# Optimization experiments

Hardware: AMD Instinct MI355X
Metric: run time of the kernel (lower is better)

Reference implementation:

```python
import jax, jax.numpy as jnp
import numpy as np

# Config: 4 sparse batch items, each with 2048 active voxels (uniform-length case
# of sparse full self-attention). channels=1024, heads=16, head_dim=64.
B_SEQ, L, H, D = 4, 2048, 16, 64
C = H * D  # 1024
N = B_SEQ * L  # 8192
EPS = 1e-12  # F.normalize eps


def setup_inputs() -> dict:
    key = jax.random.key(0)
    ks = jax.random.split(key, 6)
    s = 1.0 / np.sqrt(C)
    return {
        "x": jax.random.normal(ks[0], (N, C), dtype=jnp.float32),
        "W_qkv": jax.random.normal(ks[1], (C, 3 * C), dtype=jnp.float32) * s,
        "b_qkv": jnp.zeros((3 * C,), dtype=jnp.float32),
        "gamma_q": jnp.ones((H, D), dtype=jnp.float32),
        "gamma_k": jnp.ones((H, D), dtype=jnp.float32),
        "W_out": jax.random.normal(ks[2], (C, C), dtype=jnp.float32) * s,
        "b_out": jnp.zeros((C,), dtype=jnp.float32),
    }


def _qk_rms_norm(t, gamma):
    # SparseMultiHeadRMSNorm: L2-normalize last dim, scale by gamma[h,d] * sqrt(D)
    norm = jnp.maximum(jnp.linalg.norm(t, axis=-1, keepdims=True), EPS)
    return (t / norm) * gamma * (D ** 0.5)


def reference(x, W_qkv, b_qkv, gamma_q, gamma_k, W_out, b_out):
    qkv = x @ W_qkv + b_qkv                       # [N, 3C]
    qkv = qkv.reshape(B_SEQ, L, 3, H, D)          # fused pre-reshape
    q, k, v = qkv[:, :, 0], qkv[:, :, 1], qkv[:, :, 2]  # [B,L,H,D]
    q = _qk_rms_norm(q, gamma_q)
    k = _qk_rms_norm(k, gamma_k)
    # full scaled dot-product attention within each sparse batch item
    scores = jnp.einsum('blhd,bmhd->bhlm', q, k) / (D ** 0.5)
    attn = jax.nn.softmax(scores, axis=-1)
    h = jnp.einsum('bhlm,bmhd->blhd', attn, v)    # [B,L,H,D]
    h = h.reshape(N, C)
    return h @ W_out + b_out
```

## Files before the change

### kernel.cpp

```cpp
#include <hip/hip_runtime.h>

using u16 = unsigned short;

typedef float  f32x4  __attribute__((ext_vector_type(4)));
typedef float  f32x16 __attribute__((ext_vector_type(16)));
typedef __bf16 bf16x8 __attribute__((ext_vector_type(8)));
typedef short  s16x8  __attribute__((ext_vector_type(8)));

#define DEVI __device__ __forceinline__

constexpr int TOK = 8192;
constexpr int CIN = 1024;
constexpr int C3  = 3072;
constexpr int NH  = 16;
constexpr int HD  = 64;
constexpr int SL  = 2048;
constexpr int BH  = 64;

constexpr float LOG2E = 1.4426950408889634f;

DEVI u16 f2bf(float x) {
  unsigned u = __builtin_bit_cast(unsigned, x);
  u += 0x7FFFu + ((u >> 16) & 1u);
  return (u16)(u >> 16);
}

DEVI f32x4 mfma16(s16x8 a, s16x8 b, f32x4 c) {
  return __builtin_amdgcn_mfma_f32_16x16x32_bf16(
      __builtin_bit_cast(bf16x8, a), __builtin_bit_cast(bf16x8, b), c, 0, 0, 0);
}

DEVI f32x16 mfma32(s16x8 a, s16x8 b, f32x16 c) {
  return __builtin_amdgcn_mfma_f32_32x32x16_bf16(
      __builtin_bit_cast(bf16x8, a), __builtin_bit_cast(bf16x8, b), c, 0, 0, 0);
}

DEVI void gload_lds16(const void* g, void* l) {
  __builtin_amdgcn_global_load_lds(
      (const __attribute__((address_space(1))) unsigned int*)g,
      (__attribute__((address_space(3))) unsigned int*)l, 16, 0, 0);
}

DEVI unsigned cvtpk(float lo, float hi) {
  unsigned r;
  asm("v_cvt_pk_bf16_f32 %0, %1, %2" : "=v"(r) : "v"(lo), "v"(hi));
  return r;
}

DEVI void plswap(unsigned& a, unsigned& b) {
  asm("v_permlane32_swap_b32 %0, %1" : "+v"(a), "+v"(b));
}

DEVI void do_transpose(const float* __restrict__ in, u16* __restrict__ out,
                       int R, int C, int blk, int tid, u16 (*t)[72]) {
  int rt = R >> 6;
  int tr = (blk % rt) << 6;
  int tc = (blk / rt) << 6;
#pragma unroll
  for (int k2 = 0; k2 < 16; k2++) {
    int idx = k2 * 256 + tid;
    int r = idx >> 6, c = idx & 63;
    t[r][c] = f2bf(in[(size_t)(tr + r) * C + tc + c]);
  }
  __syncthreads();
#pragma unroll
  for (int k2 = 0; k2 < 16; k2++) {
    int idx = k2 * 256 + tid;
    int r = idx >> 6, c = idx & 63;
    out[(size_t)(tc + r) * R + tr + c] = t[c][r];
  }
}

__global__ __launch_bounds__(256) void k_prep(
    const float* __restrict__ x, u16* __restrict__ xb,
    const float* __restrict__ Wqkv, u16* __restrict__ wqT,
    const float* __restrict__ Wout, u16* __restrict__ woT,
    const float* __restrict__ gq, const float* __restrict__ gk,
    float* __restrict__ bnd) {
  __shared__ u16 t[64][72];
  const int bid = blockIdx.x, tid = threadIdx.x;
  if (bid < 1024) {
    const int total = TOK * CIN / 4;
    for (int i = bid * 256 + tid; i < total; i += 1024 * 256) {
      float4 v = ((const float4*)x)[i];
      ushort4 o;
      o.x = f2bf(v.x); o.y = f2bf(v.y); o.z = f2bf(v.z); o.w = f2bf(v.w);
      ((ushort4*)xb)[i] = o;
    }
  } else if (bid < 1024 + 768) {
    do_transpose(Wqkv, wqT, 1024, 3072, bid - 1024, tid, t);
  } else if (bid < 1024 + 768 + 256) {
    do_transpose(Wout, woT, 1024, 1024, bid - 1792, tid, t);
  } else {
    const int h = tid >> 4, s = tid & 15;
    float mv = 0.f;
#pragma unroll
    for (int j = 0; j < 4; j++) {
      int d = s * 4 + j;
      mv = fmaxf(mv, fabsf(gq[h * 64 + d] * gk[h * 64 + d]));
    }
    mv = fmaxf(mv, __shfl_xor(mv, 1));
    mv = fmaxf(mv, __shfl_xor(mv, 2));
    mv = fmaxf(mv, __shfl_xor(mv, 4));
    mv = fmaxf(mv, __shfl_xor(mv, 8));
    if (s == 0) bnd[h] = 8.0f * LOG2E * mv;
  }
}

#define STAGE6(BUF, KT)                                                  \
  { char* Ld = L + (BUF) * 49152;                                        \
    const size_t ko = (size_t)(KT) * 128;                                \
    gload_lds16(Ab + ko,          Ld + wb);                              \
    gload_lds16(Ab + ko + 131072, Ld + 8192 + wb);                       \
    gload_lds16(Ab + ko + 262144, Ld + 16384 + wb);                      \
    gload_lds16(Ab + ko + 393216, Ld + 24576 + wb);                      \
    gload_lds16(Bb + ko,          Ld + 32768 + wb);                      \
    gload_lds16(Bb + ko + 131072, Ld + 40960 + wb); }

#define KBODY(KT, DOSTAGE, VMSTR)                                        \
  {                                                                      \
    if (DOSTAGE) STAGE6(((KT) + 2) % 3, (KT) + 2)                        \
    asm volatile("s_waitcnt " VMSTR ::: "memory");                       \
    __builtin_amdgcn_s_barrier();                                        \
    const char* Lb = L + ((KT) % 3) * 49152;                             \
    s16x8 af[4][2], bfr[4][2];                                           \
    _Pragma("unroll")                                                    \
    for (int mf = 0; mf < 4; mf++) {                                     \
      af[mf][0] = *(const s16x8*)(Lb + aoff + mf * 2048 + cx0);          \
      af[mf][1] = *(const s16x8*)(Lb + aoff + mf * 2048 + (cx0 ^ 64));   \
    }                                                                    \
    _Pragma("unroll")                                                    \
    for (int nf = 0; nf < 4; nf++) {                                     \
      bfr[nf][0] = *(const s16x8*)(Lb + boff + nf * 2048 + cx0);         \
      bfr[nf][1] = *(const s16x8*)(Lb + boff + nf * 2048 + (cx0 ^ 64));  \
    }                                                                    \
    __builtin_amdgcn_s_setprio(1);                                       \
    _Pragma("unroll")                                                    \
    for (int ks = 0; ks < 2; ks++)                                       \
      _Pragma("unroll")                                                  \
      for (int mf = 0; mf < 4; mf++)                                     \
        _Pragma("unroll")                                                \
        for (int nf = 0; nf < 4; nf++)                                   \
          acc[mf][nf] = mfma16(af[mf][ks], bfr[nf][ks], acc[mf][nf]);    \
    __builtin_amdgcn_s_setprio(0);                                       \
    __builtin_amdgcn_s_barrier();                                        \
  }

DEVI void gemm_mainloop(const char* Ab, const char* Bb, char* L,
                        int wb, int aoff, int boff, int cx0,
                        f32x4 (&acc)[4][4]) {
  STAGE6(0, 0)
  STAGE6(1, 1)
#pragma unroll
  for (int kt = 0; kt < 14; ++kt) KBODY(kt, 1, "vmcnt(12)")
  KBODY(14, 0, "vmcnt(6)")
  KBODY(15, 0, "vmcnt(0)")
}

__global__ __launch_bounds__(512, 2) void k_gemm_qkv(
    const u16* __restrict__ A, const u16* __restrict__ Bt,
    const float* __restrict__ bias, const float* __restrict__ gq,
    const float* __restrict__ gk,
    u16* __restrict__ Qn, u16* __restrict__ Kn, u16* __restrict__ Vt) {
  __shared__ __align__(16) char Lsh[3][49152];
  int bid = blockIdx.x;
  bid = (bid & 7) * 96 + (bid >> 3);
  const int bm = (bid / 24) * 256, bn = (bid % 24) * 128;
  const int tid = threadIdx.x, lane = tid & 63, w = tid >> 6;
  const int l15 = lane & 15, g = lane >> 4;
  const int wr4 = w >> 1, wc2 = w & 1;

  const int rA  = tid >> 3;
  const int scb = ((tid & 7) << 4) ^ ((rA & 7) << 4);
  const char* Ab = (const char*)A + (size_t)(bm + rA) * 2048 + scb;
  const char* Bb = (const char*)Bt + (size_t)(bn + rA) * 2048 + scb;
  const int wb   = w << 10;
  const int aoff = (wr4 * 64 + l15) * 128;
  const int boff = 32768 + (wc2 * 64 + l15) * 128;
  const int cx0  = (g ^ (l15 & 7)) << 4;

  f32x4 acc[4][4];
#pragma unroll
  for (int i = 0; i < 4; i++)
#pragma unroll
    for (int j = 0; j < 4; j++) acc[i][j] = f32x4{0.f, 0.f, 0.f, 0.f};

  gemm_mainloop(Ab, Bb, (char*)Lsh, wb, aoff, boff, cx0, acc);

  const int c0 = bn + wc2 * 64;
  const int sec = c0 >> 10;
  const int head = (c0 & 1023) >> 6;
  float bv[4], gv[4];
#pragma unroll
  for (int nf = 0; nf < 4; nf++) {
    bv[nf] = bias[c0 + nf * 16 + l15];
    gv[nf] = 1.f;
    if (sec == 0) gv[nf] = gq[head * 64 + nf * 16 + l15];
    if (sec == 1) gv[nf] = gk[head * 64 + nf * 16 + l15];
  }
#pragma unroll
  for (int mf = 0; mf < 4; mf++) {
#pragma unroll
    for (int nf = 0; nf < 4; nf++)
#pragma unroll
      for (int r = 0; r < 4; r++) acc[mf][nf][r] += bv[nf];
    if (sec < 2) {
#pragma unroll
      for (int r = 0; r < 4; r++) {
        float ss = 0.f;
#pragma unroll
        for (int nf = 0; nf < 4; nf++) ss += acc[mf][nf][r] * acc[mf][nf][r];
        ss += __shfl_xor(ss, 1); ss += __shfl_xor(ss, 2);
        ss += __shfl_xor(ss, 4); ss += __shfl_xor(ss, 8);
        float nrm = fmaxf(sqrtf(ss), 1e-12f);
        float f = (sec == 0 ? LOG2E : 8.0f) / nrm;
#pragma unroll
        for (int nf = 0; nf < 4; nf++) acc[mf][nf][r] *= f;
      }
    }
    int rbase = bm + wr4 * 64 + mf * 16 + 4 * g;
#pragma unroll
    for (int r = 0; r < 4; r++) {
      int row = rbase + r;
      int b = row >> 11, tok = row & 2047;
      int bh = b * NH + head;
#pragma unroll
      for (int nf = 0; nf < 4; nf++) {
        int d = nf * 16 + l15;
        u16 val = f2bf(acc[mf][nf][r] * gv[nf]);
        if (sec == 0)      Qn[((size_t)bh * SL + tok) * HD + d] = val;
        else if (sec == 1) Kn[((size_t)bh * SL + tok) * HD + d] = val;
        else               Vt[((size_t)bh * HD + d) * SL + tok] = val;
      }
    }
  }
}

__global__ __launch_bounds__(512, 2) void k_gemm_out(
    const u16* __restrict__ A, const u16* __restrict__ Bt,
    const float* __restrict__ bias, float* __restrict__ out) {
  __shared__ __align__(16) char Lsh[3][49152];
  int bid = blockIdx.x;
  bid = (bid & 7) * 32 + (bid >> 3);
  const int bm = (bid / 8) * 256, bn = (bid % 8) * 128;
  const int tid = threadIdx.x, lane = tid & 63, w = tid >> 6;
  const int l15 = lane & 15, g = lane >> 4;
  const int wr4 = w >> 1, wc2 = w & 1;

  const int rA  = tid >> 3;
  const int scb = ((tid & 7) << 4) ^ ((rA & 7) << 4);
  const char* Ab = (const char*)A + (size_t)(bm + rA) * 2048 + scb;
  const char* Bb = (const char*)Bt + (size_t)(bn + rA) * 2048 + scb;
  const int wb   = w << 10;
  const int aoff = (wr4 * 64 + l15) * 128;
  const int boff = 32768 + (wc2 * 64 + l15) * 128;
  const int cx0  = (g ^ (l15 & 7)) << 4;

  f32x4 acc[4][4];
#pragma unroll
  for (int i = 0; i < 4; i++)
#pragma unroll
    for (int j = 0; j < 4; j++) acc[i][j] = f32x4{0.f, 0.f, 0.f, 0.f};

  gemm_mainloop(Ab, Bb, (char*)Lsh, wb, aoff, boff, cx0, acc);

  float bv[4];
#pragma unroll
  for (int nf = 0; nf < 4; nf++) bv[nf] = bias[bn + wc2 * 64 + nf * 16 + l15];
#pragma unroll
  for (int mf = 0; mf < 4; mf++)
#pragma unroll
    for (int r = 0; r < 4; r++) {
      int row = bm + wr4 * 64 + mf * 16 + 4 * g + r;
#pragma unroll
      for (int nf = 0; nf < 4; nf++)
        out[(size_t)row * CIN + bn + wc2 * 64 + nf * 16 + l15] =
            acc[mf][nf][r] + bv[nf];
    }
}

__global__ __launch_bounds__(512) void k_attn(const u16* __restrict__ Qn,
                                              const u16* __restrict__ Kn,
                                              const u16* __restrict__ Vt,
                                              const float* __restrict__ bnd,
                                              u16* __restrict__ hm) {
  __shared__ __align__(16) char KL[2][8192];
  __shared__ __align__(16) char VL[2][8192];
  const int bh = blockIdx.x & 63, qb = blockIdx.x >> 6;
  const int tid = threadIdx.x, w = tid >> 6, lane = tid & 63;
  const int l31 = lane & 31, h = lane >> 5;
  const int qr0 = qb * 256 + w * 32;
  const float negM = -bnd[bh & 15];

  const int sr  = tid >> 3;
  const int scb = ((tid & 7) << 4) ^ ((sr & 7) << 4);
  const char* kst = (const char*)(Kn + (size_t)bh * SL * HD) + (size_t)sr * 128 + scb;
  const char* vst = (const char*)(Vt + (size_t)bh * HD * SL) + (size_t)sr * 4096 + scb;
  char* kl0 = KL[0] + (w << 10);
  char* vl0 = VL[0] + (w << 10);
  char* kl1 = KL[1] + (w << 10);
  char* vl1 = VL[1] + (w << 10);

  const u16* Qb = Qn + ((size_t)bh * SL + qr0 + l31) * HD + 8 * h;
  s16x8 qf[4];
#pragma unroll
  for (int ks = 0; ks < 4; ks++) qf[ks] = *(const s16x8*)(Qb + ks * 16);

  const int lb = l31 * 128 + ((h << 4) ^ ((l31 & 7) << 4));

  f32x16 o0, o1;
#pragma unroll
  for (int i = 0; i < 16; i++) { o0[i] = 0.f; o1[i] = 0.f; }
  float lr = 0.f;

  gload_lds16(kst, kl0);
  gload_lds16(vst, vl0);
  __syncthreads();

  for (int it = 0; it < 32; ++it) {
    const char* KB = (it & 1) ? KL[1] : KL[0];
    const char* VB = (it & 1) ? VL[1] : VL[0];
    if (it < 31) {
      const size_t ko = (size_t)(it + 1) << 13;
      const size_t vo = (size_t)(it + 1) << 7;
      gload_lds16(kst + ko, (it & 1) ? kl0 : kl1);
      gload_lds16(vst + vo, (it & 1) ? vl0 : vl1);
    }

    f32x16 s0, s1;
#pragma unroll
    for (int i = 0; i < 16; i++) { s0[i] = negM; s1[i] = negM; }
    __builtin_amdgcn_s_setprio(1);
#pragma unroll
    for (int ks = 0; ks < 4; ks++) {
      const s16x8 ka  = *(const s16x8*)(KB + (lb ^ (ks << 5)));
      const s16x8 kb2 = *(const s16x8*)(KB + 4096 + (lb ^ (ks << 5)));
      s0 = mfma32(ka, qf[ks], s0);
      s1 = mfma32(kb2, qf[ks], s1);
    }
    __builtin_amdgcn_s_setprio(0);

#pragma unroll
    for (int i = 0; i < 16; i++) s0[i] = __builtin_amdgcn_exp2f(s0[i]);
#pragma unroll
    for (int i = 0; i < 16; i++) s1[i] = __builtin_amdgcn_exp2f(s1[i]);
    float sm8[8];
#pragma unroll
    for (int i = 0; i < 8; i++)
      sm8[i] = (s0[i] + s0[i + 8]) + (s1[i] + s1[i + 8]);
    lr += ((sm8[0] + sm8[1]) + (sm8[2] + sm8[3])) +
          ((sm8[4] + sm8[5]) + (sm8[6] + sm8[7]));

    union PBu { unsigned u[4]; s16x8 v; } pb;
#define MK_PB(SV, B)                              \
    {                                             \
      unsigned a0 = cvtpk(SV[B + 0], SV[B + 1]);  \
      unsigned c0 = cvtpk(SV[B + 4], SV[B + 5]);  \
      plswap(a0, c0);                             \
      unsigned a1 = cvtpk(SV[B + 2], SV[B + 3]);  \
      unsigned c1 = cvtpk(SV[B + 6], SV[B + 7]);  \
      plswap(a1, c1);                             \
      pb.u[0] = a0; pb.u[1] = a1; pb.u[2] = c0; pb.u[3] = c1; \
    }
#define PV_STEP(KS)                                            \
    {                                                          \
      const s16x8 va = *(const s16x8*)(VB + (lb ^ (KS << 5))); \
      const s16x8 vb = *(const s16x8*)(VB + 4096 + (lb ^ (KS << 5))); \
      __builtin_amdgcn_s_setprio(1);                           \
      o0 = mfma32(va, pb.v, o0);                               \
      o1 = mfma32(vb, pb.v, o1);                               \
      __builtin_amdgcn_s_setprio(0);                           \
    }
    MK_PB(s0, 0) PV_STEP(0)
    MK_PB(s0, 8) PV_STEP(1)
    MK_PB(s1, 0) PV_STEP(2)
    MK_PB(s1, 8) PV_STEP(3)
#undef MK_PB
#undef PV_STEP

    __syncthreads();
  }

  const float ltot = lr + __shfl_xor(lr, 32);
  const float inv = 1.f / ltot;
  const int bq = bh >> 4, hh = bh & 15;
  u16* hb = hm + ((size_t)bq * SL + qr0 + l31) * CIN + hh * HD;
#pragma unroll
  for (int rg = 0; rg < 4; rg++) {
    const int d0 = 8 * rg + 4 * h;
    unsigned lo = cvtpk(o0[4 * rg + 0] * inv, o0[4 * rg + 1] * inv);
    unsigned hi = cvtpk(o0[4 * rg + 2] * inv, o0[4 * rg + 3] * inv);
    *(unsigned long long*)(hb + d0) =
        (unsigned long long)lo | ((unsigned long long)hi << 32);
    unsigned lo1 = cvtpk(o1[4 * rg + 0] * inv, o1[4 * rg + 1] * inv);
    unsigned hi1 = cvtpk(o1[4 * rg + 2] * inv, o1[4 * rg + 3] * inv);
    *(unsigned long long*)(hb + 32 + d0) =
        (unsigned long long)lo1 | ((unsigned long long)hi1 << 32);
  }
}

extern "C" void kernel_launch(void* const* d_in, const int* in_sizes, int n_in,
                              void* d_out, int out_size, void* d_ws, size_t ws_size,
                              hipStream_t stream) {
  const float* x    = (const float*)d_in[0];
  const float* Wqkv = (const float*)d_in[1];
  const float* bqkv = (const float*)d_in[2];
  const float* gq   = (const float*)d_in[3];
  const float* gk   = (const float*)d_in[4];
  const float* Wout = (const float*)d_in[5];
  const float* bout = (const float*)d_in[6];
  float* out = (float*)d_out;

  char* ws = (char*)d_ws;
  u16* xb  = (u16*)(ws);
  u16* wqT = (u16*)(ws + 16777216);
  u16* woT = (u16*)(ws + 23068672);
  u16* Qn  = (u16*)(ws + 25165824);
  u16* Kn  = (u16*)(ws + 41943040);
  u16* Vt  = (u16*)(ws + 58720256);
  u16* hm  = (u16*)(ws + 75497472);
  float* bnd = (float*)(ws + 92274688);

  k_prep<<<2049, 256, 0, stream>>>(x, xb, Wqkv, wqT, Wout, woT, gq, gk, bnd);
  k_gemm_qkv<<<(TOK / 256) * (C3 / 128), 512, 0, stream>>>(xb, wqT, bqkv, gq, gk, Qn, Kn, Vt);
  k_attn<<<BH * (SL / 256), 512, 0, stream>>>(Qn, Kn, Vt, bnd, hm);
  k_gemm_out<<<(TOK / 256) * (CIN / 128), 512, 0, stream>>>(hm, woT, bout, out);
}
```

Baseline: 199.5 us.

## Triple-buffer K/V tiles in attention with explicit vmcnt waits and barriers

```diff
diff --git a/kernel.cpp b/kernel.cpp
--- a/kernel.cpp
+++ b/kernel.cpp
@@ -284,8 +284,8 @@
                                               const u16* __restrict__ Vt,
                                               const float* __restrict__ bnd,
                                               u16* __restrict__ hm) {
-  __shared__ __align__(16) char KL[2][8192];
-  __shared__ __align__(16) char VL[2][8192];
+  __shared__ __align__(16) char KL[3][8192];
+  __shared__ __align__(16) char VL[3][8192];
   const int bh = blockIdx.x & 63, qb = blockIdx.x >> 6;
   const int tid = threadIdx.x, w = tid >> 6, lane = tid & 63;
   const int l31 = lane & 31, h = lane >> 5;
@@ -296,10 +296,7 @@
   const int scb = ((tid & 7) << 4) ^ ((sr & 7) << 4);
   const char* kst = (const char*)(Kn + (size_t)bh * SL * HD) + (size_t)sr * 128 + scb;
   const char* vst = (const char*)(Vt + (size_t)bh * HD * SL) + (size_t)sr * 4096 + scb;
-  char* kl0 = KL[0] + (w << 10);
-  char* vl0 = VL[0] + (w << 10);
-  char* kl1 = KL[1] + (w << 10);
-  char* vl1 = VL[1] + (w << 10);
+  const int kwoff = w << 10;
 
   const u16* Qb = Qn + ((size_t)bh * SL + qr0 + l31) * HD + 8 * h;
   s16x8 qf[4];
@@ -313,45 +310,47 @@
   for (int i = 0; i < 16; i++) { o0[i] = 0.f; o1[i] = 0.f; }
   float lr = 0.f;
 
-  gload_lds16(kst, kl0);
-  gload_lds16(vst, vl0);
-  __syncthreads();
-
-  for (int it = 0; it < 32; ++it) {
-    const char* KB = (it & 1) ? KL[1] : KL[0];
-    const char* VB = (it & 1) ? VL[1] : VL[0];
-    if (it < 31) {
-      const size_t ko = (size_t)(it + 1) << 13;
-      const size_t vo = (size_t)(it + 1) << 7;
-      gload_lds16(kst + ko, (it & 1) ? kl0 : kl1);
-      gload_lds16(vst + vo, (it & 1) ? vl0 : vl1);
-    }
-
-    f32x16 s0, s1;
-#pragma unroll
-    for (int i = 0; i < 16; i++) { s0[i] = negM; s1[i] = negM; }
-    __builtin_amdgcn_s_setprio(1);
-#pragma unroll
-    for (int ks = 0; ks < 4; ks++) {
-      const s16x8 ka  = *(const s16x8*)(KB + (lb ^ (ks << 5)));
-      const s16x8 kb2 = *(const s16x8*)(KB + 4096 + (lb ^ (ks << 5)));
-      s0 = mfma32(ka, qf[ks], s0);
-      s1 = mfma32(kb2, qf[ks], s1);
-    }
-    __builtin_amdgcn_s_setprio(0);
-
-#pragma unroll
-    for (int i = 0; i < 16; i++) s0[i] = __builtin_amdgcn_exp2f(s0[i]);
-#pragma unroll
-    for (int i = 0; i < 16; i++) s1[i] = __builtin_amdgcn_exp2f(s1[i]);
-    float sm8[8];
-#pragma unroll
-    for (int i = 0; i < 8; i++)
-      sm8[i] = (s0[i] + s0[i + 8]) + (s1[i] + s1[i + 8]);
-    lr += ((sm8[0] + sm8[1]) + (sm8[2] + sm8[3])) +
-          ((sm8[4] + sm8[5]) + (sm8[6] + sm8[7]));
-
-    union PBu { unsigned u[4]; s16x8 v; } pb;
+#define ATT_STAGE(SLOT, T)                                          \
+  { gload_lds16(kst + ((size_t)(T) << 13), KL[SLOT] + kwoff);       \
+    gload_lds16(vst + ((size_t)(T) << 7),  VL[SLOT] + kwoff); }
+
+#define ATT_BODY(T, DOSTAGE, VMSTR)                                           \
+  {                                                                           \
+    if (DOSTAGE) ATT_STAGE(((T) + 2) % 3, (T) + 2)                            \
+    asm volatile("s_waitcnt " VMSTR ::: "memory");                            \
+    __builtin_amdgcn_s_barrier();                                             \
+    const char* KB = KL[(T) % 3];                                             \
+    const char* VB = VL[(T) % 3];                                             \
+    f32x16 s0, s1;                                                            \
+    _Pragma("unroll")                                                         \
+    for (int i = 0; i < 16; i++) { s0[i] = negM; s1[i] = negM; }              \
+    __builtin_amdgcn_s_setprio(1);                                            \
+    _Pragma("unroll")                                                         \
+    for (int ks = 0; ks < 4; ks++) {                                          \
+      const s16x8 ka  = *(const s16x8*)(KB + (lb ^ (ks << 5)));               \
+      const s16x8 kb2 = *(const s16x8*)(KB + 4096 + (lb ^ (ks << 5)));        \
+      s0 = mfma32(ka, qf[ks], s0);                                            \
+      s1 = mfma32(kb2, qf[ks], s1);                                           \
+    }                                                                         \
+    __builtin_amdgcn_s_setprio(0);                                            \
+    _Pragma("unroll")                                                         \
+    for (int i = 0; i < 16; i++) s0[i] = __builtin_amdgcn_exp2f(s0[i]);       \
+    _Pragma("unroll")                                                         \
+    for (int i = 0; i < 16; i++) s1[i] = __builtin_amdgcn_exp2f(s1[i]);       \
+    float sm8[8];                                                             \
+    _Pragma("unroll")                                                         \
+    for (int i = 0; i < 8; i++)                                               \
+      sm8[i] = (s0[i] + s0[i + 8]) + (s1[i] + s1[i + 8]);                     \
+    lr += ((sm8[0] + sm8[1]) + (sm8[2] + sm8[3])) +                           \
+          ((sm8[4] + sm8[5]) + (sm8[6] + sm8[7]));                            \
+    union PBu { unsigned u[4]; s16x8 v; } pb;                                 \
+    MK_PB(s0, 0) PV_STEP(0)                                                   \
+    MK_PB(s0, 8) PV_STEP(1)                                                   \
+    MK_PB(s1, 0) PV_STEP(2)                                                   \
+    MK_PB(s1, 8) PV_STEP(3)                                                   \
+    __builtin_amdgcn_s_barrier();                                             \
+  }
+
 #define MK_PB(SV, B)                              \
     {                                             \
       unsigned a0 = cvtpk(SV[B + 0], SV[B + 1]);  \
@@ -371,15 +370,17 @@
       o1 = mfma32(vb, pb.v, o1);                               \
       __builtin_amdgcn_s_setprio(0);                           \
     }
-    MK_PB(s0, 0) PV_STEP(0)
-    MK_PB(s0, 8) PV_STEP(1)
-    MK_PB(s1, 0) PV_STEP(2)
-    MK_PB(s1, 8) PV_STEP(3)
+
+  ATT_STAGE(0, 0)
+  ATT_STAGE(1, 1)
+#pragma unroll 3
+  for (int t = 0; t < 30; ++t) ATT_BODY(t, 1, "vmcnt(4)")
+  ATT_BODY(30, 0, "vmcnt(2)")
+  ATT_BODY(31, 0, "vmcnt(0)")
+#undef ATT_STAGE
+#undef ATT_BODY
 #undef MK_PB
 #undef PV_STEP
-
-    __syncthreads();
-  }
 
   const float ltot = lr + __shfl_xor(lr, 32);
   const float inv = 1.f / ltot;
```

Measured after the change: 197.2 us (median of 2 runs). About the same (-1.1%).
